# Kernel tuning notes

Hardware: AMD Instinct MI355X
Metric: run time of the kernel (lower is better)

## Reference

```python
import jax, jax.numpy as jnp
import numpy as np

EMBED_DIM = 1024
NUM_HEADS = 16
HEAD_DIM = EMBED_DIM // NUM_HEADS
B, S = 2, 2048


def setup_inputs() -> dict:
    key = jax.random.key(0)
    ks = jax.random.split(key, 9)
    scale = 1.0 / np.sqrt(EMBED_DIM)
    return {
        "x": jax.random.normal(ks[0], (B, S, EMBED_DIM), dtype=jnp.float32),
        "Wq": jax.random.normal(ks[1], (EMBED_DIM, EMBED_DIM), dtype=jnp.float32) * scale,
        "bq": jnp.zeros((EMBED_DIM,), dtype=jnp.float32),
        "Wk": jax.random.normal(ks[2], (EMBED_DIM, EMBED_DIM), dtype=jnp.float32) * scale,
        "bk": jnp.zeros((EMBED_DIM,), dtype=jnp.float32),
        "Wv": jax.random.normal(ks[3], (EMBED_DIM, EMBED_DIM), dtype=jnp.float32) * scale,
        "bv": jnp.zeros((EMBED_DIM,), dtype=jnp.float32),
        "Wo": jax.random.normal(ks[4], (EMBED_DIM, EMBED_DIM), dtype=jnp.float32) * scale,
        "bo": jnp.zeros((EMBED_DIM,), dtype=jnp.float32),
    }


def _split_heads(t):
    # [B, S, E] -> [B, H, S, Dh]
    b, s, _ = t.shape
    return t.reshape(b, s, NUM_HEADS, HEAD_DIM).transpose(0, 2, 1, 3)


def reference(x, Wq, bq, Wk, bk, Wv, bv, Wo, bo):
    q = _split_heads(x @ Wq + bq)
    k = _split_heads(x @ Wk + bk)
    v = _split_heads(x @ Wv + bv)
    scale = jnp.sqrt(jnp.asarray(HEAD_DIM, dtype=x.dtype))
    scores = jnp.einsum("bhqd,bhkd->bhqk", q, k) / scale
    attn = jax.nn.softmax(scores, axis=-1)
    out = jnp.einsum("bhqk,bhkd->bhqd", attn, v)  # [B,H,S,Dh]
    out = out.transpose(0, 2, 1, 3).reshape(x.shape[0], x.shape[1], EMBED_DIM)
    return out @ Wo + bo
```

## Files before the change

kernel.cpp:

```cpp
#include <hip/hip_runtime.h>
#include <math.h>
#include <stdint.h>

typedef __bf16 bf16;
typedef __bf16 bf16x4 __attribute__((ext_vector_type(4)));
typedef __bf16 bf16x8 __attribute__((ext_vector_type(8)));
typedef float f32x4 __attribute__((ext_vector_type(4)));
typedef float f32x16 __attribute__((ext_vector_type(16)));

constexpr int E = 1024;
constexpr int S = 2048;
constexpr int H = 16;


__device__ __forceinline__ void gload16(const void* g, void* l) {
  __builtin_amdgcn_global_load_lds(
      (__attribute__((address_space(1))) void*)(uintptr_t)g,
      (__attribute__((address_space(3))) void*)(uint32_t)(uintptr_t)l, 16, 0, 0);
}

__device__ __forceinline__ f32x4 mfma16(bf16x8 a, bf16x8 b, f32x4 c) {
  return __builtin_amdgcn_mfma_f32_16x16x32_bf16(a, b, c, 0, 0, 0);
}
__device__ __forceinline__ f32x16 mfma32(bf16x8 a, bf16x8 b, f32x16 c) {
  return __builtin_amdgcn_mfma_f32_32x32x16_bf16(a, b, c, 0, 0, 0);
}
__device__ __forceinline__ void lgkm0() {
  asm volatile("s_waitcnt lgkmcnt(0)" ::: "memory");
}

__global__ __launch_bounds__(256) void cast_x(const float* __restrict__ x,
                                              bf16* __restrict__ o) {
  const size_t i = ((size_t)blockIdx.x * 256 + threadIdx.x) * 8;
  const float4 a = *(const float4*)(x + i);
  const float4 b = *(const float4*)(x + i + 4);
  bf16x8 r;
  r[0] = (bf16)a.x; r[1] = (bf16)a.y; r[2] = (bf16)a.z; r[3] = (bf16)a.w;
  r[4] = (bf16)b.x; r[5] = (bf16)b.y; r[6] = (bf16)b.z; r[7] = (bf16)b.w;
  *(bf16x8*)(o + i) = r;
}

__global__ __launch_bounds__(256) void transpose_cast_w(
    const float* __restrict__ W0, const float* __restrict__ W1,
    const float* __restrict__ W2, const float* __restrict__ W3,
    bf16* __restrict__ T0, bf16* __restrict__ T1, bf16* __restrict__ T2,
    bf16* __restrict__ T3) {
  const float* W;
  bf16* T;
  switch (blockIdx.z) {
    case 0: W = W0; T = T0; break;
    case 1: W = W1; T = T1; break;
    case 2: W = W2; T = T2; break;
    default: W = W3; T = T3; break;
  }
  __shared__ float t[64][65];
  const int k0 = blockIdx.y * 64, n0 = blockIdx.x * 64;
  const int tr = threadIdx.x >> 4;
  const int tc = (threadIdx.x & 15) * 4;
#pragma unroll
  for (int u = 0; u < 4; ++u) {
    const float4 v = *(const float4*)(W + (size_t)(k0 + tr + u * 16) * E + n0 + tc);
    t[tr + u * 16][tc + 0] = v.x;
    t[tr + u * 16][tc + 1] = v.y;
    t[tr + u * 16][tc + 2] = v.z;
    t[tr + u * 16][tc + 3] = v.w;
  }
  __syncthreads();
#pragma unroll
  for (int u = 0; u < 4; ++u) {
    const int n = tr + u * 16;
    bf16x4 o;
#pragma unroll
    for (int i = 0; i < 4; ++i) o[i] = (bf16)t[tc + i][n];
    *(bf16x4*)(T + (size_t)(n0 + n) * E + k0 + tc) = o;
  }
}

__global__ __launch_bounds__(256) void gemm_qkv(const bf16* __restrict__ A,
                                                const bf16* __restrict__ Wt,
                                                const float* __restrict__ bq,
                                                const float* __restrict__ bk,
                                                const float* __restrict__ bv,
                                                bf16* __restrict__ qo,
                                                bf16* __restrict__ ko,
                                                bf16* __restrict__ vo) {
  __shared__ __attribute__((aligned(16))) bf16 Asm[128 * 32];
  __shared__ __attribute__((aligned(16))) bf16 Bsm[128 * 32];
  const int z = blockIdx.z;
  const bf16* Bt = Wt + (size_t)z * E * E;
  const float* bias = (z == 0) ? bq : (z == 1) ? bk : bv;
  const int tid = threadIdx.x;
  const int w = tid >> 6, lane = tid & 63, quad = lane >> 4, ln = lane & 15;
  const int bm = blockIdx.y * 128, bn = blockIdx.x * 128;
  const int wr = w >> 1, wc = w & 1;
  const int srow = w * 32 + (lane >> 2);
  const int scol = (lane & 3) * 8;
  const bf16* Ag = A + (size_t)(bm + srow) * E + scol;
  const bf16* Bg = Bt + (size_t)(bn + srow) * E + scol;
  f32x4 acc[4][4] = {};

  for (int k0 = 0; k0 < E; k0 += 32) {
    gload16(Ag + k0, &Asm[(w * 32) * 32]);
    gload16(Ag + k0 + (size_t)16 * E, &Asm[(w * 32 + 16) * 32]);
    gload16(Bg + k0, &Bsm[(w * 32) * 32]);
    gload16(Bg + k0 + (size_t)16 * E, &Bsm[(w * 32 + 16) * 32]);
    __syncthreads();
    bf16x8 af[4], bfr[4];
#pragma unroll
    for (int t = 0; t < 4; ++t) {
      af[t] = *(const bf16x8*)&Asm[(wr * 64 + t * 16 + ln) * 32 + quad * 8];
      bfr[t] = *(const bf16x8*)&Bsm[(wc * 64 + t * 16 + ln) * 32 + quad * 8];
    }
#pragma unroll
    for (int rt = 0; rt < 4; ++rt)
#pragma unroll
      for (int ct = 0; ct < 4; ++ct)
        acc[rt][ct] = mfma16(af[rt], bfr[ct], acc[rt][ct]);
    __syncthreads();
  }

  const float scl = (z == 0) ? 0.125f : 1.0f;
  const int hglob = (bn + wc * 64) >> 6;
  float bvv[4];
#pragma unroll
  for (int ct = 0; ct < 4; ++ct) bvv[ct] = bias[bn + wc * 64 + ct * 16 + ln];

#pragma unroll
  for (int rt = 0; rt < 4; ++rt) {
    const int row0 = bm + wr * 64 + rt * 16 + quad * 4;
    const int bb = row0 >> 11;
    const int rl = row0 & 2047;
    const size_t hb = (size_t)(bb * 16 + hglob) * 131072;
#pragma unroll
    for (int ct = 0; ct < 4; ++ct) {
      if (z == 2) {
        const int mt = ct >> 1, ln32 = ((ct & 1) << 4) | ln;
        const int tau = rl >> 6, hfv = (rl >> 3) & 1, j0 = rl & 7;
        bf16x4 p;
#pragma unroll
        for (int r = 0; r < 4; ++r) p[r] = (bf16)(acc[rt][ct][r] + bvv[ct]);
        *(bf16x4*)&vo[hb + (size_t)((tau * 8 + mt * 4 + rt) * 512 +
                                    hfv * 256 + ln32 * 8 + j0)] = p;
      } else {
        bf16* o = (z == 0) ? qo : ko;
        const int t = rl >> 5, ln0 = rl & 31;
        const size_t base =
            hb + (size_t)((t * 4 + ct) * 512 + (ln >> 3) * 256 + (ln & 7));
#pragma unroll
        for (int r = 0; r < 4; ++r)
          o[base + (ln0 + r) * 8] = (bf16)((acc[rt][ct][r] + bvv[ct]) * scl);
      }
    }
  }
}

__global__ __launch_bounds__(256) void gemm_wo(const bf16* __restrict__ A,
                                               const bf16* __restrict__ Bt,
                                               const float* __restrict__ bias,
                                               float* __restrict__ C) {
  __shared__ __attribute__((aligned(16))) bf16 Asm[64 * 32];
  __shared__ __attribute__((aligned(16))) bf16 Bsm[128 * 32];
  const int tid = threadIdx.x;
  const int w = tid >> 6, lane = tid & 63, quad = lane >> 4, ln = lane & 15;
  const int bm = blockIdx.y * 64, bn = blockIdx.x * 128;
  const int wr = w >> 1, wc = w & 1;
  const int sr = lane >> 2, sc = (lane & 3) * 8;
  const bf16* Ag = A + (size_t)(bm + w * 16 + sr) * E + sc;
  const bf16* Bg = Bt + (size_t)(bn + w * 32 + sr) * E + sc;
  f32x4 acc[2][4] = {};

  for (int k0 = 0; k0 < E; k0 += 32) {
    gload16(Ag + k0, &Asm[(w * 16) * 32]);
    gload16(Bg + k0, &Bsm[(w * 32) * 32]);
    gload16(Bg + k0 + (size_t)16 * E, &Bsm[(w * 32 + 16) * 32]);
    __syncthreads();
    bf16x8 af[2], bfr[4];
#pragma unroll
    for (int t = 0; t < 2; ++t)
      af[t] = *(const bf16x8*)&Asm[(wr * 32 + t * 16 + ln) * 32 + quad * 8];
#pragma unroll
    for (int t = 0; t < 4; ++t)
      bfr[t] = *(const bf16x8*)&Bsm[(wc * 64 + t * 16 + ln) * 32 + quad * 8];
#pragma unroll
    for (int rt = 0; rt < 2; ++rt)
#pragma unroll
      for (int ct = 0; ct < 4; ++ct)
        acc[rt][ct] = mfma16(af[rt], bfr[ct], acc[rt][ct]);
    __syncthreads();
  }

  float bvv[4];
#pragma unroll
  for (int ct = 0; ct < 4; ++ct) bvv[ct] = bias[bn + wc * 64 + ct * 16 + ln];
#pragma unroll
  for (int rt = 0; rt < 2; ++rt) {
    const int row0 = bm + wr * 32 + rt * 16 + quad * 4;
#pragma unroll
    for (int ct = 0; ct < 4; ++ct) {
      const int c = bn + wc * 64 + ct * 16 + ln;
#pragma unroll
      for (int r = 0; r < 4; ++r)
        C[(size_t)(row0 + r) * E + c] = acc[rt][ct][r] + bvv[ct];
    }
  }
}

__global__ __launch_bounds__(512, 4) void attn_mfma(const bf16* __restrict__ Qf,
                                                    const bf16* __restrict__ Kf,
                                                    const bf16* __restrict__ Vf,
                                                    bf16* __restrict__ Og) {
  __shared__ __attribute__((aligned(16))) char smem[49152];
  bf16* KsB = (bf16*)smem;
  bf16* VsB = (bf16*)(smem + 16384);
  bf16* PlB = (bf16*)(smem + 32768);

  const int tid = threadIdx.x;
  const int w = tid >> 6, lane = tid & 63, ln = lane & 31, hf = lane >> 5;
  const int qi = w & 3, ki = w >> 2;
  const int tq = blockIdx.x * 4 + qi;
  const int h = blockIdx.y, b = blockIdx.z;
  const size_t fb = (size_t)(b * H + h) * 131072;

  bf16x8 qf[4];
  {
    const bf16* qb = Qf + fb + (size_t)tq * 2048 + lane * 8;
#pragma unroll
    for (int c = 0; c < 4; ++c) qf[c] = *(const bf16x8*)(qb + c * 512);
  }

  bf16* Ks = KsB + ki * 4096;
  bf16* Vs = VsB + ki * 4096;
  bf16* Pw = PlB + w * 1024;

  const bf16* Ksrc = Kf + fb + qi * 1024 + lane * 8;
  const bf16* Vsrc = Vf + fb + qi * 1024 + lane * 8;
  bf16* Kdst = Ks + qi * 1024;
  bf16* Vdst = Vs + qi * 1024;

  float lpart = 0.f;
  f32x16 oacc[2] = {};

  for (int i = 0; i < 16; ++i) {
    const size_t toff = (size_t)(ki * 16 + i) * 4096;
    gload16(Ksrc + toff, Kdst);
    gload16(Ksrc + toff + 512, Kdst + 512);
    gload16(Vsrc + toff, Vdst);
    gload16(Vsrc + toff + 512, Vdst + 512);
    __syncthreads();

#pragma unroll
    for (int mt = 0; mt < 2; ++mt) {
      f32x16 st = {};
#pragma unroll
      for (int c = 0; c < 4; ++c)
        st = mfma32(*(const bf16x8*)&Ks[(mt * 4 + c) * 512 + lane * 8], qf[c], st);

#pragma unroll
      for (int g = 0; g < 4; ++g) {
        bf16x4 pk;
#pragma unroll
        for (int j = 0; j < 4; ++j) {
          const float p = __expf(st[g * 4 + j]);
          lpart += p;
          pk[j] = (bf16)p;
        }
        *(bf16x4*)&Pw[g * 256 + ln * 8 + hf * 4] = pk;
      }
      lgkm0();

      const bf16x8 pb0 = *(const bf16x8*)&Pw[lane * 8];
      const bf16x8 pb1 = *(const bf16x8*)&Pw[512 + lane * 8];
      lgkm0();

#pragma unroll
      for (int vt = 0; vt < 2; ++vt) {
        oacc[vt] = mfma32(
            *(const bf16x8*)&Vs[(vt * 4 + mt * 2 + 0) * 512 + lane * 8], pb0,
            oacc[vt]);
        oacc[vt] = mfma32(
            *(const bf16x8*)&Vs[(vt * 4 + mt * 2 + 1) * 512 + lane * 8], pb1,
            oacc[vt]);
      }
    }
    __syncthreads();
  }

  float* Ocmb = (float*)smem;
  float* Lcmb = (float*)(smem + 32768);
  if (ki == 1) {
#pragma unroll
    for (int vt = 0; vt < 2; ++vt)
#pragma unroll
      for (int r = 0; r < 16; ++r)
        Ocmb[qi * 2048 + (vt * 16 + r) * 64 + lane] = oacc[vt][r];
    Lcmb[qi * 64 + lane] = lpart;
  }
  __syncthreads();
  if (ki == 0) {
#pragma unroll
    for (int vt = 0; vt < 2; ++vt)
#pragma unroll
      for (int r = 0; r < 16; ++r)
        oacc[vt][r] += Ocmb[qi * 2048 + (vt * 16 + r) * 64 + lane];
    lpart += Lcmb[qi * 64 + lane];

    lpart += __shfl_xor(lpart, 32);
    const float inv = 1.0f / lpart;

    bf16* orow = Og + ((size_t)b * S + (size_t)tq * 32 + ln) * E + h * 64;
#pragma unroll
    for (int vt = 0; vt < 2; ++vt) {
#pragma unroll
      for (int g = 0; g < 4; ++g) {
        bf16x4 o;
#pragma unroll
        for (int j = 0; j < 4; ++j) o[j] = (bf16)(oacc[vt][g * 4 + j] * inv);
        *(bf16x4*)&orow[vt * 32 + g * 8 + hf * 4] = o;
      }
    }
  }
}

extern "C" void kernel_launch(void* const* d_in, const int* in_sizes, int n_in,
                              void* d_out, int out_size, void* d_ws, size_t ws_size,
                              hipStream_t stream) {
  const float* x = (const float*)d_in[0];
  const float* Wq = (const float*)d_in[1];
  const float* bq = (const float*)d_in[2];
  const float* Wk = (const float*)d_in[3];
  const float* bk = (const float*)d_in[4];
  const float* Wv = (const float*)d_in[5];
  const float* bv = (const float*)d_in[6];
  const float* Wo = (const float*)d_in[7];
  const float* bo = (const float*)d_in[8];

  const size_t ME = (size_t)4096 * 1024;
  const size_t WE = (size_t)1024 * 1024;
  bf16* xb = (bf16*)d_ws;
  bf16* wqt = xb + ME;
  bf16* wkt = wqt + WE;
  bf16* wvt = wkt + WE;
  bf16* wot = wvt + WE;
  bf16* qb = wot + WE;
  bf16* kb = qb + ME;
  bf16* vt = kb + ME;
  bf16* ab = vt + ME;

  cast_x<<<2048, 256, 0, stream>>>(x, xb);
  transpose_cast_w<<<dim3(16, 16, 4), 256, 0, stream>>>(Wq, Wk, Wv, Wo, wqt, wkt,
                                                        wvt, wot);
  gemm_qkv<<<dim3(8, 32, 3), 256, 0, stream>>>(xb, wqt, bq, bk, bv, qb, kb, vt);
  attn_mfma<<<dim3(S / 128, H, 2), 512, 0, stream>>>(qb, kb, vt, ab);
  gemm_wo<<<dim3(8, 64), 256, 0, stream>>>(ab, wot, bo, (float*)d_out);
}
```

Baseline: 190.3 us.

## Double-buffer K/V tiles, keep P in registers via permlane swap, use exp2

The attention kernel now double-buffers K/V tiles in a 64KB LDS region, issuing the next tile's async loads before computing on the current one. Softmax probabilities are packed to bf16 and rearranged across lane halves with permlane32_swap instead of a round trip through LDS. The Q scale folds in log2(e) so exp2f replaces __expf. The larger LDS footprint may cut the number of resident blocks per CU under launch_bounds(512,4).

```diff
diff --git a/kernel.cpp b/kernel.cpp
--- a/kernel.cpp
+++ b/kernel.cpp
@@ -3,6 +3,7 @@
 #include <stdint.h>
 
 typedef __bf16 bf16;
+typedef __bf16 bf16x2 __attribute__((ext_vector_type(2)));
 typedef __bf16 bf16x4 __attribute__((ext_vector_type(4)));
 typedef __bf16 bf16x8 __attribute__((ext_vector_type(8)));
 typedef float f32x4 __attribute__((ext_vector_type(4)));
@@ -25,8 +26,12 @@
 __device__ __forceinline__ f32x16 mfma32(bf16x8 a, bf16x8 b, f32x16 c) {
   return __builtin_amdgcn_mfma_f32_32x32x16_bf16(a, b, c, 0, 0, 0);
 }
-__device__ __forceinline__ void lgkm0() {
-  asm volatile("s_waitcnt lgkmcnt(0)" ::: "memory");
+
+__device__ __forceinline__ uint32_t pkbf(float lo, float hi) {
+  bf16x2 p;
+  p[0] = (bf16)lo;
+  p[1] = (bf16)hi;
+  return __builtin_bit_cast(uint32_t, p);
 }
 
 __global__ __launch_bounds__(256) void cast_x(const float* __restrict__ x,
@@ -119,7 +124,7 @@
     __syncthreads();
   }
 
-  const float scl = (z == 0) ? 0.125f : 1.0f;
+  const float scl = (z == 0) ? 0.18033688f : 1.0f;
   const int hglob = (bn + wc * 64) >> 6;
   float bvv[4];
 #pragma unroll
@@ -209,10 +214,7 @@
                                                     const bf16* __restrict__ Kf,
                                                     const bf16* __restrict__ Vf,
                                                     bf16* __restrict__ Og) {
-  __shared__ __attribute__((aligned(16))) char smem[49152];
-  bf16* KsB = (bf16*)smem;
-  bf16* VsB = (bf16*)(smem + 16384);
-  bf16* PlB = (bf16*)(smem + 32768);
+  __shared__ __attribute__((aligned(16))) char smem[65536];
 
   const int tid = threadIdx.x;
   const int w = tid >> 6, lane = tid & 63, ln = lane & 31, hf = lane >> 5;
@@ -228,62 +230,82 @@
     for (int c = 0; c < 4; ++c) qf[c] = *(const bf16x8*)(qb + c * 512);
   }
 
-  bf16* Ks = KsB + ki * 4096;
-  bf16* Vs = VsB + ki * 4096;
-  bf16* Pw = PlB + w * 1024;
-
   const bf16* Ksrc = Kf + fb + qi * 1024 + lane * 8;
   const bf16* Vsrc = Vf + fb + qi * 1024 + lane * 8;
-  bf16* Kdst = Ks + qi * 1024;
-  bf16* Vdst = Vs + qi * 1024;
+  const int dstoff = ki * 4096 + qi * 1024;
 
   float lpart = 0.f;
   f32x16 oacc[2] = {};
 
+#define STAGE(i, buf)                                                  \
+  do {                                                                 \
+    const size_t toff = (size_t)(ki * 16 + (i)) * 4096;                \
+    bf16* kd = (bf16*)(smem + (buf) * 32768) + dstoff;                 \
+    bf16* vd = (bf16*)(smem + (buf) * 32768 + 16384) + dstoff;         \
+    gload16(Ksrc + toff, kd);                                          \
+    gload16(Ksrc + toff + 512, kd + 512);                              \
+    gload16(Vsrc + toff, vd);                                          \
+    gload16(Vsrc + toff + 512, vd + 512);                              \
+  } while (0)
+
+  STAGE(0, 0);
+  __syncthreads();
+
+#pragma unroll 2
   for (int i = 0; i < 16; ++i) {
-    const size_t toff = (size_t)(ki * 16 + i) * 4096;
-    gload16(Ksrc + toff, Kdst);
-    gload16(Ksrc + toff + 512, Kdst + 512);
-    gload16(Vsrc + toff, Vdst);
-    gload16(Vsrc + toff + 512, Vdst + 512);
-    __syncthreads();
+    const int cur = i & 1;
+    if (i < 15) STAGE(i + 1, cur ^ 1);
+    const bf16* Ks = (const bf16*)(smem + cur * 32768) + ki * 4096;
+    const bf16* Vs = (const bf16*)(smem + cur * 32768 + 16384) + ki * 4096;
 
 #pragma unroll
     for (int mt = 0; mt < 2; ++mt) {
       f32x16 st = {};
 #pragma unroll
       for (int c = 0; c < 4; ++c)
-        st = mfma32(*(const bf16x8*)&Ks[(mt * 4 + c) * 512 + lane * 8], qf[c], st);
-
-#pragma unroll
-      for (int g = 0; g < 4; ++g) {
-        bf16x4 pk;
-#pragma unroll
-        for (int j = 0; j < 4; ++j) {
-          const float p = __expf(st[g * 4 + j]);
-          lpart += p;
-          pk[j] = (bf16)p;
-        }
-        *(bf16x4*)&Pw[g * 256 + ln * 8 + hf * 4] = pk;
-      }
-      lgkm0();
-
-      const bf16x8 pb0 = *(const bf16x8*)&Pw[lane * 8];
-      const bf16x8 pb1 = *(const bf16x8*)&Pw[512 + lane * 8];
-      lgkm0();
+        st = mfma32(*(const bf16x8*)&Ks[(mt * 4 + c) * 512 + lane * 8], qf[c],
+                    st);
+
+      float pe[16];
+#pragma unroll
+      for (int r = 0; r < 16; ++r) {
+        pe[r] = exp2f(st[r]);
+        lpart += pe[r];
+      }
+
+      bf16x8 pb[2];
+#pragma unroll
+      for (int cl = 0; cl < 2; ++cl) {
+        uint32_t a01 = pkbf(pe[cl * 8 + 0], pe[cl * 8 + 1]);
+        uint32_t a23 = pkbf(pe[cl * 8 + 2], pe[cl * 8 + 3]);
+        uint32_t b01 = pkbf(pe[cl * 8 + 4], pe[cl * 8 + 5]);
+        uint32_t b23 = pkbf(pe[cl * 8 + 6], pe[cl * 8 + 7]);
+        auto r0 = __builtin_amdgcn_permlane32_swap(a01, b01, false, false);
+        auto r1 = __builtin_amdgcn_permlane32_swap(a23, b23, false, false);
+        union {
+          bf16x8 v;
+          uint32_t u[4];
+        } pu;
+        pu.u[0] = r0[0];
+        pu.u[1] = r1[0];
+        pu.u[2] = r0[1];
+        pu.u[3] = r1[1];
+        pb[cl] = pu.v;
+      }
 
 #pragma unroll
       for (int vt = 0; vt < 2; ++vt) {
         oacc[vt] = mfma32(
-            *(const bf16x8*)&Vs[(vt * 4 + mt * 2 + 0) * 512 + lane * 8], pb0,
+            *(const bf16x8*)&Vs[(vt * 4 + mt * 2 + 0) * 512 + lane * 8], pb[0],
             oacc[vt]);
         oacc[vt] = mfma32(
-            *(const bf16x8*)&Vs[(vt * 4 + mt * 2 + 1) * 512 + lane * 8], pb1,
+            *(const bf16x8*)&Vs[(vt * 4 + mt * 2 + 1) * 512 + lane * 8], pb[1],
             oacc[vt]);
       }
     }
     __syncthreads();
   }
+#undef STAGE
 
   float* Ocmb = (float*)smem;
   float* Lcmb = (float*)(smem + 32768);
```

Result: slower. 198.8 us (+4.4%).
